# Optimization experiments

Hardware: AMD Instinct MI355X
Metric: run time of the kernel (lower is better)

## Reference

```python
import jax, jax.numpy as jnp
import numpy as np

N_NODES = 100000
N_EDGES = 3200000
F_IN, F_HID, F_OUT = 512, 128, 32


def setup_inputs() -> dict:
    key = jax.random.key(0)
    ks = jax.random.split(key, 8)
    x = jax.random.normal(ks[0], (N_NODES, F_IN), dtype=jnp.float32)
    edge_row = jax.random.randint(ks[1], (N_EDGES,), 0, N_NODES, dtype=jnp.int32)
    edge_col = jax.random.randint(ks[2], (N_EDGES,), 0, N_NODES, dtype=jnp.int32)
    edge_val = jax.random.uniform(ks[3], (N_EDGES,), dtype=jnp.float32)
    W1 = jax.random.normal(ks[4], (F_IN, F_HID), dtype=jnp.float32) / np.sqrt(F_IN)
    b1 = jnp.zeros((F_HID,), dtype=jnp.float32)
    W2 = jax.random.normal(ks[5], (F_HID, F_OUT), dtype=jnp.float32) / np.sqrt(F_HID)
    b2 = jnp.zeros((F_OUT,), dtype=jnp.float32)
    return {"x": x, "edge_row": edge_row, "edge_col": edge_col,
            "edge_val": edge_val, "W1": W1, "b1": b1, "W2": W2, "b2": b2}


def _spmm(edge_row, edge_col, edge_val, dense):
    # out[r] = sum_{e: row[e]==r} val[e] * dense[col[e]]  (COO SpMM)
    gathered = dense[edge_col] * edge_val[:, None]  # [E, F]
    return jax.ops.segment_sum(gathered, edge_row, num_segments=N_NODES)


def reference(x, edge_row, edge_col, edge_val, W1, b1, W2, b2):
    # GraphConvolution 1: support = x@W1; out = A @ support + b1
    h = _spmm(edge_row, edge_col, edge_val, x @ W1) + b1
    h = jax.nn.relu(h)
    # GraphConvolution 2
    logits = _spmm(edge_row, edge_col, edge_val, h @ W2) + b2
    return jax.nn.log_softmax(logits, axis=1)
```

## Files before the change

### kernel.cpp

```cpp
#include <hip/hip_runtime.h>


#define NN 100000
#define NE 3200000
#define FIN 512
#define FHID 128
#define FOUT 32
#define BROWS 256
#define NBUCK 391
#define NPART 256
#define CHUNK 12800
#define TOT (NBUCK * NPART)
#define NSCAN1 98

typedef __attribute__((ext_vector_type(8))) short bf16x8;
typedef __attribute__((ext_vector_type(4))) float f32x4;

static __device__ __forceinline__ unsigned short f2bf(float f) {
    unsigned u = __float_as_uint(f);
    unsigned r = (u + 0x7FFFu + ((u >> 16) & 1u)) >> 16;
    return (unsigned short)r;
}
static __device__ __forceinline__ float bf2f(unsigned short u) {
    return __uint_as_float(((unsigned)u) << 16);
}
static __device__ __forceinline__ float bflo(unsigned u) {
    return __uint_as_float(u << 16);
}
static __device__ __forceinline__ float bfhi(unsigned u) {
    return __uint_as_float(u & 0xffff0000u);
}

__global__ __launch_bounds__(256) void hist_part(const int* __restrict__ erow,
                                                 int* __restrict__ cntG) {
    __shared__ int c[NBUCK];
    const int t = threadIdx.x;
    const int w = blockIdx.x;
    for (int i = t; i < NBUCK; i += 256) c[i] = 0;
    __syncthreads();
    const int e0 = w * CHUNK;
    const int e1 = min(e0 + CHUNK, NE);
    for (int e = e0 + t; e < e1; e += 256) atomicAdd(&c[erow[e] >> 8], 1);
    __syncthreads();
    for (int i = t; i < NBUCK; i += 256) cntG[w * NBUCK + i] = c[i];
}

__global__ __launch_bounds__(256) void scan1_kernel(const int* __restrict__ cntG,
                                                    int* __restrict__ off,
                                                    int* __restrict__ partials) {
    __shared__ int s[256];
    int t = threadIdx.x;
    int i0 = blockIdx.x * 1024 + t * 4;
    int v[4];
#pragma unroll
    for (int j = 0; j < 4; ++j) {
        int i = i0 + j;
        v[j] = (i < TOT) ? cntG[(i & (NPART - 1)) * NBUCK + (i >> 8)] : 0;
    }
    int lsum = v[0] + v[1] + v[2] + v[3];
    s[t] = lsum;
    __syncthreads();
    for (int o = 1; o < 256; o <<= 1) {
        int xv = (t >= o) ? s[t - o] : 0;
        __syncthreads();
        s[t] += xv;
        __syncthreads();
    }
    if (t == 255) partials[blockIdx.x] = s[255];
    int run = s[t] - lsum;
#pragma unroll
    for (int j = 0; j < 4; ++j) {
        if (i0 + j < TOT) off[i0 + j] = run;
        run += v[j];
    }
}

__global__ void scan2_kernel(int* partials) {
    __shared__ int s[128];
    int t = threadIdx.x;
    int v = (t < NSCAN1) ? partials[t] : 0;
    s[t] = v;
    __syncthreads();
    for (int o = 1; o < 128; o <<= 1) {
        int xv = (t >= o) ? s[t - o] : 0;
        __syncthreads();
        s[t] += xv;
        __syncthreads();
    }
    if (t < NSCAN1) partials[t] = s[t] - v;
}

__global__ __launch_bounds__(256) void scan3_kernel(int* __restrict__ off,
                                                    const int* __restrict__ partials) {
    int add = partials[blockIdx.x];
    int i0 = blockIdx.x * 1024 + threadIdx.x * 4;
#pragma unroll
    for (int j = 0; j < 4; ++j)
        if (i0 + j < TOT) off[i0 + j] += add;
}

__global__ void make_bstart(const int* __restrict__ off, int* __restrict__ bstart) {
    int t = blockIdx.x * 256 + threadIdx.x;
    if (t < NBUCK) bstart[t] = off[t * NPART];
    if (t == 0) bstart[NBUCK] = NE;
}

__global__ __launch_bounds__(256) void scatter_part(const int* __restrict__ erow,
                                                    const int* __restrict__ ecol,
                                                    const float* __restrict__ eval,
                                                    const int* __restrict__ off,
                                                    int2* __restrict__ bcolval) {
    __shared__ int pos[NBUCK];
    const int t = threadIdx.x;
    const int w = blockIdx.x;
    for (int b = t; b < NBUCK; b += 256) pos[b] = off[b * NPART + w];
    __syncthreads();
    const int e0 = w * CHUNK;
    const int e1 = min(e0 + CHUNK, NE);
    for (int e = e0 + t; e < e1; e += 256) {
        int r = erow[e];
        int idx = atomicAdd(&pos[r >> 8], 1);
        bcolval[idx] = make_int2(ecol[e] | ((r & 255) << 20), __float_as_int(eval[e]));
    }
}

__global__ __launch_bounds__(256) void bucket_to_csr(const int* __restrict__ bstart,
                                                     const int2* __restrict__ bcolval,
                                                     int* __restrict__ rowptr,
                                                     int2* __restrict__ epack) {
    __shared__ int cnt[256];
    __shared__ int pos[256];
    __shared__ int s[256];
    const int b = blockIdx.x;
    const int t = threadIdx.x;
    const int s0 = bstart[b];
    const int n = bstart[b + 1] - s0;
    cnt[t] = 0;
    __syncthreads();
    for (int i = t; i < n; i += 256)
        atomicAdd(&cnt[((unsigned)bcolval[s0 + i].x) >> 20], 1);
    __syncthreads();
    int myc = cnt[t];
    s[t] = myc;
    __syncthreads();
    for (int o = 1; o < 256; o <<= 1) {
        int xv = (t >= o) ? s[t - o] : 0;
        __syncthreads();
        s[t] += xv;
        __syncthreads();
    }
    int excl = s[t] - myc;
    pos[t] = excl;
    int row = b * BROWS + t;
    if (row < NN) rowptr[row] = s0 + excl;
    if (b == 0 && t == 0) rowptr[NN] = NE;
    __syncthreads();
    for (int i = t; i < n; i += 256) {
        int2 v = bcolval[s0 + i];
        int p = atomicAdd(&pos[((unsigned)v.x) >> 20], 1);
        epack[s0 + p] = make_int2(v.x & 0xFFFFF, v.y);
    }
}

__global__ __launch_bounds__(256) void prep_w1(const float* __restrict__ W1,
                                               unsigned short* __restrict__ W1t) {
    int t = blockIdx.x * 256 + threadIdx.x;
    int n = t & 127;
    int k = t >> 7;
    W1t[n * 512 + k] = f2bf(W1[k * 128 + n]);
}

__global__ __launch_bounds__(256) void gemm1_mfma(const float* __restrict__ x,
                                                  const unsigned short* __restrict__ W1t,
                                                  unsigned short* __restrict__ out) {
    __shared__ __align__(16) unsigned short As[128 * 32];
    const int tid = threadIdx.x;
    const int lane = tid & 63;
    const int w = __builtin_amdgcn_readfirstlane(tid >> 6);
    const int quad = lane >> 4;
    const int m = lane & 15;
    const int row0 = blockIdx.x * 128;

    f32x4 acc[8][2];
#pragma unroll
    for (int mt = 0; mt < 8; ++mt)
#pragma unroll
        for (int nt = 0; nt < 2; ++nt) acc[mt][nt] = (f32x4){0.f, 0.f, 0.f, 0.f};

    int srow[4], skq[4];
    const float* sptr[4];
#pragma unroll
    for (int s = 0; s < 4; ++s) {
        int f = tid + s * 256;
        srow[s] = f >> 3;
        skq[s] = f & 7;
        sptr[s] = x + (size_t)(row0 + srow[s]) * FIN + skq[s] * 4;
    }
    float4 ld[4];
#pragma unroll
    for (int s = 0; s < 4; ++s)
        ld[s] = (row0 + srow[s] < NN) ? *(const float4*)sptr[s]
                                      : make_float4(0.f, 0.f, 0.f, 0.f);

    for (int ks = 0; ks < 16; ++ks) {
        __syncthreads();
#pragma unroll
        for (int s = 0; s < 4; ++s) {
            int r = srow[s], kq = skq[s];
            int mt = r >> 4, mm = r & 15;
            int off = mt * 512 + (kq >> 1) * 128 + mm * 8 + (kq & 1) * 4;
            ushort4 p;
            p.x = f2bf(ld[s].x);
            p.y = f2bf(ld[s].y);
            p.z = f2bf(ld[s].z);
            p.w = f2bf(ld[s].w);
            *(ushort4*)&As[off] = p;
        }
        __syncthreads();
        if (ks < 15) {
#pragma unroll
            for (int s = 0; s < 4; ++s)
                ld[s] = (row0 + srow[s] < NN)
                            ? *(const float4*)(sptr[s] + (ks + 1) * 32)
                            : make_float4(0.f, 0.f, 0.f, 0.f);
        }
        bf16x8 bfr[2];
#pragma unroll
        for (int nt = 0; nt < 2; ++nt) {
            int n = (w * 2 + nt) * 16 + m;
            bfr[nt] = *(const bf16x8*)(W1t + (size_t)n * 512 + ks * 32 + quad * 8);
        }
#pragma unroll
        for (int mt = 0; mt < 8; ++mt) {
            bf16x8 af = *(const bf16x8*)&As[mt * 512 + quad * 128 + m * 8];
            acc[mt][0] = __builtin_amdgcn_mfma_f32_16x16x32_bf16(af, bfr[0], acc[mt][0], 0, 0, 0);
            acc[mt][1] = __builtin_amdgcn_mfma_f32_16x16x32_bf16(af, bfr[1], acc[mt][1], 0, 0, 0);
        }
    }
#pragma unroll
    for (int mt = 0; mt < 8; ++mt)
#pragma unroll
        for (int nt = 0; nt < 2; ++nt) {
            int col = (w * 2 + nt) * 16 + m;
#pragma unroll
            for (int r = 0; r < 4; ++r) {
                int row = row0 + mt * 16 + quad * 4 + r;
                if (row < NN) out[(size_t)row * FHID + col] = f2bf(acc[mt][nt][r]);
            }
        }
}

__global__ __launch_bounds__(256) void spmm1_kernel(const int* __restrict__ rowptr,
                                                    const int2* __restrict__ epack,
                                                    const unsigned short* __restrict__ dense,
                                                    const float* __restrict__ b1,
                                                    unsigned short* __restrict__ h) {
    const int gtid = blockIdx.x * 256 + threadIdx.x;
    const int wid = gtid >> 6;
    const int lane = threadIdx.x & 63;
    const int q = lane >> 4;
    const int sl = lane & 15;
    const int row = wid * 4 + q;
    const int start = rowptr[row];
    const int cnt = rowptr[row + 1] - start;
    float acc[8];
#pragma unroll
    for (int i = 0; i < 8; ++i) acc[i] = 0.f;

    for (int base = 0; base < cnt; base += 16) {
        const int rem = cnt - base;
        int2 p = make_int2(0, 0);
        if (sl < rem) p = epack[start + base + sl];
        const int jn = min(16, rem);
        for (int j = 0; j < jn; j += 4) {
            int cj[4];
            float vj[4];
            uint4 d[4];
#pragma unroll
            for (int k = 0; k < 4; ++k) {
                cj[k] = __shfl(p.x, q * 16 + j + k, 64);
                vj[k] = __shfl(__int_as_float(p.y), q * 16 + j + k, 64);
            }
#pragma unroll
            for (int k = 0; k < 4; ++k)
                d[k] = *(const uint4*)(dense + (size_t)cj[k] * FHID + sl * 8);
#pragma unroll
            for (int k = 0; k < 4; ++k) {
                acc[0] += vj[k] * bflo(d[k].x);
                acc[1] += vj[k] * bfhi(d[k].x);
                acc[2] += vj[k] * bflo(d[k].y);
                acc[3] += vj[k] * bfhi(d[k].y);
                acc[4] += vj[k] * bflo(d[k].z);
                acc[5] += vj[k] * bfhi(d[k].z);
                acc[6] += vj[k] * bflo(d[k].w);
                acc[7] += vj[k] * bfhi(d[k].w);
            }
        }
    }
    float4 bb0 = *(const float4*)(b1 + sl * 8);
    float4 bb1 = *(const float4*)(b1 + sl * 8 + 4);
    uint4 st;
    st.x = (unsigned)f2bf(fmaxf(acc[0] + bb0.x, 0.f)) |
           ((unsigned)f2bf(fmaxf(acc[1] + bb0.y, 0.f)) << 16);
    st.y = (unsigned)f2bf(fmaxf(acc[2] + bb0.z, 0.f)) |
           ((unsigned)f2bf(fmaxf(acc[3] + bb0.w, 0.f)) << 16);
    st.z = (unsigned)f2bf(fmaxf(acc[4] + bb1.x, 0.f)) |
           ((unsigned)f2bf(fmaxf(acc[5] + bb1.y, 0.f)) << 16);
    st.w = (unsigned)f2bf(fmaxf(acc[6] + bb1.z, 0.f)) |
           ((unsigned)f2bf(fmaxf(acc[7] + bb1.w, 0.f)) << 16);
    *(uint4*)(h + (size_t)row * FHID + sl * 8) = st;
}

__global__ __launch_bounds__(256) void gemm2_kernel(const unsigned short* __restrict__ h,
                                                    const float* __restrict__ W2,
                                                    unsigned short* __restrict__ out) {
    __shared__ float hs[64][129];
    const int tid = threadIdx.x;
    const int lane = tid & 63;
    const int cg = __builtin_amdgcn_readfirstlane(tid >> 6);
    const int row0 = blockIdx.x * 64;
    const int row = row0 + lane;

    float acc[8];
#pragma unroll
    for (int c = 0; c < 8; ++c) acc[c] = 0.f;

#pragma unroll
    for (int j = 0; j < 8; ++j) {
        int f4 = tid + j * 256;
        int r = f4 >> 5;
        int kq = f4 & 31;
        ushort4 v = make_ushort4(0, 0, 0, 0);
        if (row0 + r < NN) v = *(const ushort4*)(h + (size_t)(row0 + r) * FHID + kq * 4);
        hs[r][kq * 4 + 0] = bf2f(v.x);
        hs[r][kq * 4 + 1] = bf2f(v.y);
        hs[r][kq * 4 + 2] = bf2f(v.z);
        hs[r][kq * 4 + 3] = bf2f(v.w);
    }
    __syncthreads();
#pragma unroll 4
    for (int k = 0; k < FHID; ++k) {
        float a = hs[lane][k];
        const float* wrow = W2 + k * FOUT + cg * 8;
#pragma unroll
        for (int c = 0; c < 8; ++c) acc[c] += a * wrow[c];
    }
    if (row < NN) {
        uint4 st;
        st.x = (unsigned)f2bf(acc[0]) | ((unsigned)f2bf(acc[1]) << 16);
        st.y = (unsigned)f2bf(acc[2]) | ((unsigned)f2bf(acc[3]) << 16);
        st.z = (unsigned)f2bf(acc[4]) | ((unsigned)f2bf(acc[5]) << 16);
        st.w = (unsigned)f2bf(acc[6]) | ((unsigned)f2bf(acc[7]) << 16);
        *(uint4*)(out + (size_t)row * FOUT + cg * 8) = st;
    }
}

__global__ __launch_bounds__(256) void spmm2_kernel(const int* __restrict__ rowptr,
                                                    const int2* __restrict__ epack,
                                                    const unsigned short* __restrict__ dense,
                                                    const float* __restrict__ b2,
                                                    float* __restrict__ out) {
    const int gtid = blockIdx.x * 256 + threadIdx.x;
    const int wid = gtid >> 6;
    const int lane = threadIdx.x & 63;
    const int o = lane >> 3;
    const int sl = lane & 7;
    const int row = wid * 8 + o;
    const int start = rowptr[row];
    const int cnt = rowptr[row + 1] - start;
    float acc[4];
#pragma unroll
    for (int i = 0; i < 4; ++i) acc[i] = 0.f;

    for (int base = 0; base < cnt; base += 8) {
        const int rem = cnt - base;
        int2 p = make_int2(0, 0);
        if (sl < rem) p = epack[start + base + sl];
        const int jn = min(8, rem);
        for (int j = 0; j < jn; j += 4) {
            int cj[4];
            float vj[4];
            uint2 d[4];
#pragma unroll
            for (int k = 0; k < 4; ++k) {
                cj[k] = __shfl(p.x, o * 8 + j + k, 64);
                vj[k] = __shfl(__int_as_float(p.y), o * 8 + j + k, 64);
            }
#pragma unroll
            for (int k = 0; k < 4; ++k)
                d[k] = *(const uint2*)(dense + (size_t)cj[k] * FOUT + sl * 4);
#pragma unroll
            for (int k = 0; k < 4; ++k) {
                acc[0] += vj[k] * bflo(d[k].x);
                acc[1] += vj[k] * bfhi(d[k].x);
                acc[2] += vj[k] * bflo(d[k].y);
                acc[3] += vj[k] * bfhi(d[k].y);
            }
        }
    }
    float4 bb = *(const float4*)(b2 + sl * 4);
    acc[0] += bb.x;
    acc[1] += bb.y;
    acc[2] += bb.z;
    acc[3] += bb.w;
    float m = fmaxf(fmaxf(acc[0], acc[1]), fmaxf(acc[2], acc[3]));
#pragma unroll
    for (int mask = 4; mask >= 1; mask >>= 1) m = fmaxf(m, __shfl_xor(m, mask, 64));
    float ssum = expf(acc[0] - m) + expf(acc[1] - m) + expf(acc[2] - m) + expf(acc[3] - m);
#pragma unroll
    for (int mask = 4; mask >= 1; mask >>= 1) ssum += __shfl_xor(ssum, mask, 64);
    float lse = m + logf(ssum);
    float4 st = make_float4(acc[0] - lse, acc[1] - lse, acc[2] - lse, acc[3] - lse);
    *(float4*)(out + (size_t)row * FOUT + sl * 4) = st;
}

extern "C" void kernel_launch(void* const* d_in, const int* in_sizes, int n_in,
                              void* d_out, int out_size, void* d_ws, size_t ws_size,
                              hipStream_t stream) {
    const float* x = (const float*)d_in[0];
    const int* erow = (const int*)d_in[1];
    const int* ecol = (const int*)d_in[2];
    const float* eval = (const float*)d_in[3];
    const float* W1 = (const float*)d_in[4];
    const float* b1 = (const float*)d_in[5];
    const float* W2 = (const float*)d_in[6];
    const float* b2 = (const float*)d_in[7];
    float* out = (float*)d_out;

    char* ws = (char*)d_ws;
    size_t off_b = 0;
    auto walloc = [&](size_t bytes) -> void* {
        void* p = ws + off_b;
        off_b = (off_b + bytes + 255) & ~(size_t)255;
        return p;
    };
    int2* epack = (int2*)walloc((size_t)NE * 8);
    int* rowptr = (int*)walloc((size_t)(NN + 1) * 4);
    int* cntG = (int*)walloc((size_t)TOT * 4);
    int* off = (int*)walloc((size_t)TOT * 4);
    int* bstart = (int*)walloc((size_t)(NBUCK + 1) * 4);
    int* partials = (int*)walloc(4096);
    unsigned short* W1t = (unsigned short*)walloc((size_t)FHID * FIN * 2);
    char* uni = (char*)walloc((size_t)NN * FHID * 2 * 2);
    int2* bcolval = (int2*)uni;
    unsigned short* support1 = (unsigned short*)uni;
    unsigned short* h = (unsigned short*)(uni + (size_t)NN * FHID * 2);
    unsigned short* support2 = support1;

    prep_w1<<<256, 256, 0, stream>>>(W1, W1t);
    hist_part<<<NPART, 256, 0, stream>>>(erow, cntG);
    scan1_kernel<<<NSCAN1, 256, 0, stream>>>(cntG, off, partials);
    scan2_kernel<<<1, 128, 0, stream>>>(partials);
    scan3_kernel<<<NSCAN1, 256, 0, stream>>>(off, partials);
    make_bstart<<<2, 256, 0, stream>>>(off, bstart);
    scatter_part<<<NPART, 256, 0, stream>>>(erow, ecol, eval, off, bcolval);
    bucket_to_csr<<<NBUCK, 256, 0, stream>>>(bstart, bcolval, rowptr, epack);

    gemm1_mfma<<<(NN + 127) / 128, 256, 0, stream>>>(x, W1t, support1);
    spmm1_kernel<<<NN / 16, 256, 0, stream>>>(rowptr, epack, support1, b1, h);
    gemm2_kernel<<<(NN + 63) / 64, 256, 0, stream>>>(h, W2, support2);
    spmm2_kernel<<<NN / 32, 256, 0, stream>>>(rowptr, epack, support2, b2, out);
}
```

Before: 646.9 us.

## Fuse prep kernels, merge CSR build with GEMM1, remap SpMM to wave-per-row

Merges the W1 transpose with the edge histogram, removes make_bstart, and runs bucket_to_csr and gemm1 as one launch using disjoint block ranges so they can overlap. Both SpMM kernels now assign one wavefront per row, broadcasting edge indices with readlane and having each lane gather a narrow slice of the dense row. Workspace buffers that used to alias are now allocated separately, which the fusion needs. This trades launch count and idle time for narrower per-lane gathers, and the wave-per-row mapping may waste lanes on low-degree rows.

```diff
diff --git a/kernel.cpp b/kernel.cpp
--- a/kernel.cpp
+++ b/kernel.cpp
@@ -12,6 +12,7 @@
 #define CHUNK 12800
 #define TOT (NBUCK * NPART)
 #define NSCAN1 98
+#define GG1 ((NN + 127) / 128)
 
 typedef __attribute__((ext_vector_type(8))) short bf16x8;
 typedef __attribute__((ext_vector_type(4))) float f32x4;
@@ -31,18 +32,27 @@
     return __uint_as_float(u & 0xffff0000u);
 }
 
-__global__ __launch_bounds__(256) void hist_part(const int* __restrict__ erow,
-                                                 int* __restrict__ cntG) {
-    __shared__ int c[NBUCK];
-    const int t = threadIdx.x;
-    const int w = blockIdx.x;
-    for (int i = t; i < NBUCK; i += 256) c[i] = 0;
-    __syncthreads();
-    const int e0 = w * CHUNK;
-    const int e1 = min(e0 + CHUNK, NE);
-    for (int e = e0 + t; e < e1; e += 256) atomicAdd(&c[erow[e] >> 8], 1);
-    __syncthreads();
-    for (int i = t; i < NBUCK; i += 256) cntG[w * NBUCK + i] = c[i];
+__global__ __launch_bounds__(256) void fused_prep_hist(const float* __restrict__ W1,
+                                                       unsigned short* __restrict__ W1t,
+                                                       const int* __restrict__ erow,
+                                                       int* __restrict__ cntG) {
+    if (blockIdx.x < NPART) {
+        __shared__ int c[NBUCK];
+        const int t = threadIdx.x;
+        const int w = blockIdx.x;
+        for (int i = t; i < NBUCK; i += 256) c[i] = 0;
+        __syncthreads();
+        const int e0 = w * CHUNK;
+        const int e1 = min(e0 + CHUNK, NE);
+        for (int e = e0 + t; e < e1; e += 256) atomicAdd(&c[erow[e] >> 8], 1);
+        __syncthreads();
+        for (int i = t; i < NBUCK; i += 256) cntG[w * NBUCK + i] = c[i];
+    } else {
+        int t = (blockIdx.x - NPART) * 256 + threadIdx.x;
+        int n = t & 127;
+        int k = t >> 7;
+        W1t[n * 512 + k] = f2bf(W1[k * 128 + n]);
+    }
 }
 
 __global__ __launch_bounds__(256) void scan1_kernel(const int* __restrict__ cntG,
@@ -97,12 +107,6 @@
 #pragma unroll
     for (int j = 0; j < 4; ++j)
         if (i0 + j < TOT) off[i0 + j] += add;
-}
-
-__global__ void make_bstart(const int* __restrict__ off, int* __restrict__ bstart) {
-    int t = blockIdx.x * 256 + threadIdx.x;
-    if (t < NBUCK) bstart[t] = off[t * NPART];
-    if (t == 0) bstart[NBUCK] = NE;
 }
 
 __global__ __launch_bounds__(256) void scatter_part(const int* __restrict__ erow,
@@ -124,130 +128,122 @@
     }
 }
 
-__global__ __launch_bounds__(256) void bucket_to_csr(const int* __restrict__ bstart,
-                                                     const int2* __restrict__ bcolval,
-                                                     int* __restrict__ rowptr,
-                                                     int2* __restrict__ epack) {
-    __shared__ int cnt[256];
-    __shared__ int pos[256];
-    __shared__ int s[256];
-    const int b = blockIdx.x;
-    const int t = threadIdx.x;
-    const int s0 = bstart[b];
-    const int n = bstart[b + 1] - s0;
-    cnt[t] = 0;
-    __syncthreads();
-    for (int i = t; i < n; i += 256)
-        atomicAdd(&cnt[((unsigned)bcolval[s0 + i].x) >> 20], 1);
-    __syncthreads();
-    int myc = cnt[t];
-    s[t] = myc;
-    __syncthreads();
-    for (int o = 1; o < 256; o <<= 1) {
-        int xv = (t >= o) ? s[t - o] : 0;
-        __syncthreads();
-        s[t] += xv;
-        __syncthreads();
-    }
-    int excl = s[t] - myc;
-    pos[t] = excl;
-    int row = b * BROWS + t;
-    if (row < NN) rowptr[row] = s0 + excl;
-    if (b == 0 && t == 0) rowptr[NN] = NE;
-    __syncthreads();
-    for (int i = t; i < n; i += 256) {
-        int2 v = bcolval[s0 + i];
-        int p = atomicAdd(&pos[((unsigned)v.x) >> 20], 1);
-        epack[s0 + p] = make_int2(v.x & 0xFFFFF, v.y);
-    }
-}
-
-__global__ __launch_bounds__(256) void prep_w1(const float* __restrict__ W1,
-                                               unsigned short* __restrict__ W1t) {
-    int t = blockIdx.x * 256 + threadIdx.x;
-    int n = t & 127;
-    int k = t >> 7;
-    W1t[n * 512 + k] = f2bf(W1[k * 128 + n]);
-}
-
-__global__ __launch_bounds__(256) void gemm1_mfma(const float* __restrict__ x,
-                                                  const unsigned short* __restrict__ W1t,
-                                                  unsigned short* __restrict__ out) {
-    __shared__ __align__(16) unsigned short As[128 * 32];
-    const int tid = threadIdx.x;
-    const int lane = tid & 63;
-    const int w = __builtin_amdgcn_readfirstlane(tid >> 6);
-    const int quad = lane >> 4;
-    const int m = lane & 15;
-    const int row0 = blockIdx.x * 128;
-
-    f32x4 acc[8][2];
-#pragma unroll
-    for (int mt = 0; mt < 8; ++mt)
-#pragma unroll
-        for (int nt = 0; nt < 2; ++nt) acc[mt][nt] = (f32x4){0.f, 0.f, 0.f, 0.f};
-
-    int srow[4], skq[4];
-    const float* sptr[4];
-#pragma unroll
-    for (int s = 0; s < 4; ++s) {
-        int f = tid + s * 256;
-        srow[s] = f >> 3;
-        skq[s] = f & 7;
-        sptr[s] = x + (size_t)(row0 + srow[s]) * FIN + skq[s] * 4;
-    }
-    float4 ld[4];
-#pragma unroll
-    for (int s = 0; s < 4; ++s)
-        ld[s] = (row0 + srow[s] < NN) ? *(const float4*)sptr[s]
-                                      : make_float4(0.f, 0.f, 0.f, 0.f);
-
-    for (int ks = 0; ks < 16; ++ks) {
-        __syncthreads();
+__global__ __launch_bounds__(256) void fused_csr_gemm1(
+    const int* __restrict__ off, const int2* __restrict__ bcolval,
+    int* __restrict__ rowptr, int2* __restrict__ epack,
+    const float* __restrict__ x, const unsigned short* __restrict__ W1t,
+    unsigned short* __restrict__ outd) {
+    if (blockIdx.x < GG1) {
+        __shared__ __align__(16) unsigned short As[128 * 32];
+        const int tid = threadIdx.x;
+        const int lane = tid & 63;
+        const int w = __builtin_amdgcn_readfirstlane(tid >> 6);
+        const int quad = lane >> 4;
+        const int m = lane & 15;
+        const int row0 = blockIdx.x * 128;
+
+        f32x4 acc[8][2];
+#pragma unroll
+        for (int mt = 0; mt < 8; ++mt)
+#pragma unroll
+            for (int nt = 0; nt < 2; ++nt) acc[mt][nt] = (f32x4){0.f, 0.f, 0.f, 0.f};
+
+        int srow[4], skq[4];
+        const float* sptr[4];
 #pragma unroll
         for (int s = 0; s < 4; ++s) {
-            int r = srow[s], kq = skq[s];
-            int mt = r >> 4, mm = r & 15;
-            int off = mt * 512 + (kq >> 1) * 128 + mm * 8 + (kq & 1) * 4;
-            ushort4 p;
-            p.x = f2bf(ld[s].x);
-            p.y = f2bf(ld[s].y);
-            p.z = f2bf(ld[s].z);
-            p.w = f2bf(ld[s].w);
-            *(ushort4*)&As[off] = p;
-        }
-        __syncthreads();
-        if (ks < 15) {
-#pragma unroll
-            for (int s = 0; s < 4; ++s)
-                ld[s] = (row0 + srow[s] < NN)
-                            ? *(const float4*)(sptr[s] + (ks + 1) * 32)
-                            : make_float4(0.f, 0.f, 0.f, 0.f);
-        }
-        bf16x8 bfr[2];
-#pragma unroll
-        for (int nt = 0; nt < 2; ++nt) {
-            int n = (w * 2 + nt) * 16 + m;
-            bfr[nt] = *(const bf16x8*)(W1t + (size_t)n * 512 + ks * 32 + quad * 8);
-        }
-#pragma unroll
-        for (int mt = 0; mt < 8; ++mt) {
-            bf16x8 af = *(const bf16x8*)&As[mt * 512 + quad * 128 + m * 8];
-            acc[mt][0] = __builtin_amdgcn_mfma_f32_16x16x32_bf16(af, bfr[0], acc[mt][0], 0, 0, 0);
-            acc[mt][1] = __builtin_amdgcn_mfma_f32_16x16x32_bf16(af, bfr[1], acc[mt][1], 0, 0, 0);
-        }
-    }
-#pragma unroll
-    for (int mt = 0; mt < 8; ++mt)
-#pragma unroll
-        for (int nt = 0; nt < 2; ++nt) {
-            int col = (w * 2 + nt) * 16 + m;
-#pragma unroll
-            for (int r = 0; r < 4; ++r) {
-                int row = row0 + mt * 16 + quad * 4 + r;
-                if (row < NN) out[(size_t)row * FHID + col] = f2bf(acc[mt][nt][r]);
+            int f = tid + s * 256;
+            srow[s] = f >> 3;
+            skq[s] = f & 7;
+            sptr[s] = x + (size_t)(row0 + srow[s]) * FIN + skq[s] * 4;
+        }
+        float4 ld[4];
+#pragma unroll
+        for (int s = 0; s < 4; ++s)
+            ld[s] = (row0 + srow[s] < NN) ? *(const float4*)sptr[s]
+                                          : make_float4(0.f, 0.f, 0.f, 0.f);
+
+        for (int ks = 0; ks < 16; ++ks) {
+            __syncthreads();
+#pragma unroll
+            for (int s = 0; s < 4; ++s) {
+                int r = srow[s], kq = skq[s];
+                int mt = r >> 4, mm = r & 15;
+                int offs = mt * 512 + (kq >> 1) * 128 + mm * 8 + (kq & 1) * 4;
+                ushort4 p;
+                p.x = f2bf(ld[s].x);
+                p.y = f2bf(ld[s].y);
+                p.z = f2bf(ld[s].z);
+                p.w = f2bf(ld[s].w);
+                *(ushort4*)&As[offs] = p;
             }
-        }
+            __syncthreads();
+            if (ks < 15) {
+#pragma unroll
+                for (int s = 0; s < 4; ++s)
+                    ld[s] = (row0 + srow[s] < NN)
+                                ? *(const float4*)(sptr[s] + (ks + 1) * 32)
+                                : make_float4(0.f, 0.f, 0.f, 0.f);
+            }
+            bf16x8 bfr[2];
+#pragma unroll
+            for (int nt = 0; nt < 2; ++nt) {
+                int n = (w * 2 + nt) * 16 + m;
+                bfr[nt] = *(const bf16x8*)(W1t + (size_t)n * 512 + ks * 32 + quad * 8);
+            }
+#pragma unroll
+            for (int mt = 0; mt < 8; ++mt) {
+                bf16x8 af = *(const bf16x8*)&As[mt * 512 + quad * 128 + m * 8];
+                acc[mt][0] = __builtin_amdgcn_mfma_f32_16x16x32_bf16(af, bfr[0], acc[mt][0], 0, 0, 0);
+                acc[mt][1] = __builtin_amdgcn_mfma_f32_16x16x32_bf16(af, bfr[1], acc[mt][1], 0, 0, 0);
+            }
+        }
+#pragma unroll
+        for (int mt = 0; mt < 8; ++mt)
+#pragma unroll
+            for (int nt = 0; nt < 2; ++nt) {
+                int col = (w * 2 + nt) * 16 + m;
+#pragma unroll
+                for (int r = 0; r < 4; ++r) {
+                    int row = row0 + mt * 16 + quad * 4 + r;
+                    if (row < NN) outd[(size_t)row * FHID + col] = f2bf(acc[mt][nt][r]);
+                }
+            }
+    } else {
+        __shared__ int cnt[256];
+        __shared__ int pos[256];
+        __shared__ int s[256];
+        const int b = blockIdx.x - GG1;
+        const int t = threadIdx.x;
+        const int s0 = off[b * NPART];
+        const int send = (b == NBUCK - 1) ? NE : off[(b + 1) * NPART];
+        const int n = send - s0;
+        cnt[t] = 0;
+        __syncthreads();
+        for (int i = t; i < n; i += 256)
+            atomicAdd(&cnt[((unsigned)bcolval[s0 + i].x) >> 20], 1);
+        __syncthreads();
+        int myc = cnt[t];
+        s[t] = myc;
+        __syncthreads();
+        for (int o = 1; o < 256; o <<= 1) {
+            int xv = (t >= o) ? s[t - o] : 0;
+            __syncthreads();
+            s[t] += xv;
+            __syncthreads();
+        }
+        int excl = s[t] - myc;
+        pos[t] = excl;
+        int row = b * BROWS + t;
+        if (row < NN) rowptr[row] = s0 + excl;
+        if (b == 0 && t == 0) rowptr[NN] = NE;
+        __syncthreads();
+        for (int i = t; i < n; i += 256) {
+            int2 v = bcolval[s0 + i];
+            int p = atomicAdd(&pos[((unsigned)v.x) >> 20], 1);
+            epack[s0 + p] = make_int2(v.x & 0xFFFFF, v.y);
+        }
+    }
 }
 
 __global__ __launch_bounds__(256) void spmm1_kernel(const int* __restrict__ rowptr,
@@ -255,60 +251,36 @@
                                                     const unsigned short* __restrict__ dense,
                                                     const float* __restrict__ b1,
                                                     unsigned short* __restrict__ h) {
-    const int gtid = blockIdx.x * 256 + threadIdx.x;
-    const int wid = gtid >> 6;
     const int lane = threadIdx.x & 63;
-    const int q = lane >> 4;
-    const int sl = lane & 15;
-    const int row = wid * 4 + q;
-    const int start = rowptr[row];
-    const int cnt = rowptr[row + 1] - start;
-    float acc[8];
-#pragma unroll
-    for (int i = 0; i < 8; ++i) acc[i] = 0.f;
-
-    for (int base = 0; base < cnt; base += 16) {
-        const int rem = cnt - base;
-        int2 p = make_int2(0, 0);
-        if (sl < rem) p = epack[start + base + sl];
-        const int jn = min(16, rem);
-        for (int j = 0; j < jn; j += 4) {
-            int cj[4];
-            float vj[4];
-            uint4 d[4];
-#pragma unroll
-            for (int k = 0; k < 4; ++k) {
-                cj[k] = __shfl(p.x, q * 16 + j + k, 64);
-                vj[k] = __shfl(__int_as_float(p.y), q * 16 + j + k, 64);
-            }
-#pragma unroll
-            for (int k = 0; k < 4; ++k)
-                d[k] = *(const uint4*)(dense + (size_t)cj[k] * FHID + sl * 8);
-#pragma unroll
-            for (int k = 0; k < 4; ++k) {
-                acc[0] += vj[k] * bflo(d[k].x);
-                acc[1] += vj[k] * bfhi(d[k].x);
-                acc[2] += vj[k] * bflo(d[k].y);
-                acc[3] += vj[k] * bfhi(d[k].y);
-                acc[4] += vj[k] * bflo(d[k].z);
-                acc[5] += vj[k] * bfhi(d[k].z);
-                acc[6] += vj[k] * bflo(d[k].w);
-                acc[7] += vj[k] * bfhi(d[k].w);
-            }
-        }
-    }
-    float4 bb0 = *(const float4*)(b1 + sl * 8);
-    float4 bb1 = *(const float4*)(b1 + sl * 8 + 4);
-    uint4 st;
-    st.x = (unsigned)f2bf(fmaxf(acc[0] + bb0.x, 0.f)) |
-           ((unsigned)f2bf(fmaxf(acc[1] + bb0.y, 0.f)) << 16);
-    st.y = (unsigned)f2bf(fmaxf(acc[2] + bb0.z, 0.f)) |
-           ((unsigned)f2bf(fmaxf(acc[3] + bb0.w, 0.f)) << 16);
-    st.z = (unsigned)f2bf(fmaxf(acc[4] + bb1.x, 0.f)) |
-           ((unsigned)f2bf(fmaxf(acc[5] + bb1.y, 0.f)) << 16);
-    st.w = (unsigned)f2bf(fmaxf(acc[6] + bb1.z, 0.f)) |
-           ((unsigned)f2bf(fmaxf(acc[7] + bb1.w, 0.f)) << 16);
-    *(uint4*)(h + (size_t)row * FHID + sl * 8) = st;
+    const int row = blockIdx.x * 4 + (threadIdx.x >> 6);
+    const int start = __builtin_amdgcn_readfirstlane(rowptr[row]);
+    const int cnt = __builtin_amdgcn_readfirstlane(rowptr[row + 1]) - start;
+    const int sl16 = lane & 15;
+    float acc0 = 0.f, acc1 = 0.f;
+
+    for (int j = 0; j < cnt; j += 16) {
+        int idx = j + sl16;
+        idx = idx < cnt ? idx : cnt - 1;
+        const int2 p = epack[start + idx];
+        const int rem = cnt - j;
+        unsigned d[16];
+#pragma unroll
+        for (int k = 0; k < 16; ++k) {
+            int col = __builtin_amdgcn_readlane(p.x, k);
+            col = (k < rem) ? col : 0;
+            d[k] = *((const unsigned*)(dense + ((size_t)col << 7)) + lane);
+        }
+#pragma unroll
+        for (int k = 0; k < 16; ++k) {
+            float v = (k < rem) ? __int_as_float(__builtin_amdgcn_readlane(p.y, k)) : 0.f;
+            acc0 = fmaf(v, bflo(d[k]), acc0);
+            acc1 = fmaf(v, bfhi(d[k]), acc1);
+        }
+    }
+    float2 bb = *(const float2*)(b1 + lane * 2);
+    unsigned r0 = f2bf(fmaxf(acc0 + bb.x, 0.f));
+    unsigned r1 = f2bf(fmaxf(acc1 + bb.y, 0.f));
+    *((unsigned*)(h + (size_t)row * FHID) + lane) = r0 | (r1 << 16);
 }
 
 __global__ __launch_bounds__(256) void gemm2_kernel(const unsigned short* __restrict__ h,
@@ -360,58 +332,49 @@
                                                     const unsigned short* __restrict__ dense,
                                                     const float* __restrict__ b2,
                                                     float* __restrict__ out) {
-    const int gtid = blockIdx.x * 256 + threadIdx.x;
-    const int wid = gtid >> 6;
     const int lane = threadIdx.x & 63;
-    const int o = lane >> 3;
-    const int sl = lane & 7;
-    const int row = wid * 8 + o;
-    const int start = rowptr[row];
-    const int cnt = rowptr[row + 1] - start;
-    float acc[4];
-#pragma unroll
-    for (int i = 0; i < 4; ++i) acc[i] = 0.f;
-
-    for (int base = 0; base < cnt; base += 8) {
-        const int rem = cnt - base;
-        int2 p = make_int2(0, 0);
-        if (sl < rem) p = epack[start + base + sl];
-        const int jn = min(8, rem);
-        for (int j = 0; j < jn; j += 4) {
-            int cj[4];
-            float vj[4];
-            uint2 d[4];
-#pragma unroll
-            for (int k = 0; k < 4; ++k) {
-                cj[k] = __shfl(p.x, o * 8 + j + k, 64);
-                vj[k] = __shfl(__int_as_float(p.y), o * 8 + j + k, 64);
-            }
-#pragma unroll
-            for (int k = 0; k < 4; ++k)
-                d[k] = *(const uint2*)(dense + (size_t)cj[k] * FOUT + sl * 4);
-#pragma unroll
-            for (int k = 0; k < 4; ++k) {
-                acc[0] += vj[k] * bflo(d[k].x);
-                acc[1] += vj[k] * bfhi(d[k].x);
-                acc[2] += vj[k] * bflo(d[k].y);
-                acc[3] += vj[k] * bfhi(d[k].y);
-            }
-        }
-    }
-    float4 bb = *(const float4*)(b2 + sl * 4);
-    acc[0] += bb.x;
-    acc[1] += bb.y;
-    acc[2] += bb.z;
-    acc[3] += bb.w;
-    float m = fmaxf(fmaxf(acc[0], acc[1]), fmaxf(acc[2], acc[3]));
-#pragma unroll
-    for (int mask = 4; mask >= 1; mask >>= 1) m = fmaxf(m, __shfl_xor(m, mask, 64));
-    float ssum = expf(acc[0] - m) + expf(acc[1] - m) + expf(acc[2] - m) + expf(acc[3] - m);
-#pragma unroll
-    for (int mask = 4; mask >= 1; mask >>= 1) ssum += __shfl_xor(ssum, mask, 64);
+    const int row = blockIdx.x * 4 + (threadIdx.x >> 6);
+    const int start = __builtin_amdgcn_readfirstlane(rowptr[row]);
+    const int cnt = __builtin_amdgcn_readfirstlane(rowptr[row + 1]) - start;
+    const int col = lane & 31;
+    const int slot = lane >> 5;
+    const int sl16 = lane & 15;
+    float acc = 0.f;
+
+    for (int j = 0; j < cnt; j += 16) {
+        int idx = j + sl16;
+        idx = idx < cnt ? idx : cnt - 1;
+        const int2 p = epack[start + idx];
+        const int rem = cnt - j;
+        unsigned short d[8];
+        float vv[8];
+#pragma unroll
+        for (int k = 0; k < 8; ++k) {
+            int cA = __builtin_amdgcn_readlane(p.x, 2 * k);
+            int cB = __builtin_amdgcn_readlane(p.x, 2 * k + 1);
+            int ei = 2 * k + slot;
+            int c = slot ? cB : cA;
+            c = (ei < rem) ? c : 0;
+            d[k] = *(dense + (size_t)c * FOUT + col);
+            int vA = __builtin_amdgcn_readlane(p.y, 2 * k);
+            int vB = __builtin_amdgcn_readlane(p.y, 2 * k + 1);
+            float v = __int_as_float(slot ? vB : vA);
+            vv[k] = (ei < rem) ? v : 0.f;
+        }
+#pragma unroll
+        for (int k = 0; k < 8; ++k) acc = fmaf(vv[k], bf2f(d[k]), acc);
+    }
+    acc += __shfl_xor(acc, 32, 64);
+    acc += b2[col];
+    float m = acc;
+#pragma unroll
+    for (int mask = 16; mask >= 1; mask >>= 1) m = fmaxf(m, __shfl_xor(m, mask, 64));
+    float ex = expf(acc - m);
+    float ssum = ex;
+#pragma unroll
+    for (int mask = 16; mask >= 1; mask >>= 1) ssum += __shfl_xor(ssum, mask, 64);
     float lse = m + logf(ssum);
-    float4 st = make_float4(acc[0] - lse, acc[1] - lse, acc[2] - lse, acc[3] - lse);
-    *(float4*)(out + (size_t)row * FOUT + sl * 4) = st;
+    if (lane < 32) out[(size_t)row * FOUT + col] = acc - lse;
 }
 
 extern "C" void kernel_launch(void* const* d_in, const int* in_sizes, int n_in,
@@ -438,26 +401,21 @@
     int* rowptr = (int*)walloc((size_t)(NN + 1) * 4);
     int* cntG = (int*)walloc((size_t)TOT * 4);
     int* off = (int*)walloc((size_t)TOT * 4);
-    int* bstart = (int*)walloc((size_t)(NBUCK + 1) * 4);
     int* partials = (int*)walloc(4096);
     unsigned short* W1t = (unsigned short*)walloc((size_t)FHID * FIN * 2);
-    char* uni = (char*)walloc((size_t)NN * FHID * 2 * 2);
-    int2* bcolval = (int2*)uni;
-    unsigned short* support1 = (unsigned short*)uni;
-    unsigned short* h = (unsigned short*)(uni + (size_t)NN * FHID * 2);
+    int2* bcolval = (int2*)walloc((size_t)NE * 8);
+    unsigned short* support1 = (unsigned short*)walloc((size_t)NN * FHID * 2);
+    unsigned short* h = (unsigned short*)walloc((size_t)NN * FHID * 2);
     unsigned short* support2 = support1;
 
-    prep_w1<<<256, 256, 0, stream>>>(W1, W1t);
-    hist_part<<<NPART, 256, 0, stream>>>(erow, cntG);
+    fused_prep_hist<<<NPART + 256, 256, 0, stream>>>(W1, W1t, erow, cntG);
     scan1_kernel<<<NSCAN1, 256, 0, stream>>>(cntG, off, partials);
     scan2_kernel<<<1, 128, 0, stream>>>(partials);
     scan3_kernel<<<NSCAN1, 256, 0, stream>>>(off, partials);
-    make_bstart<<<2, 256, 0, stream>>>(off, bstart);
     scatter_part<<<NPART, 256, 0, stream>>>(erow, ecol, eval, off, bcolval);
-    bucket_to_csr<<<NBUCK, 256, 0, stream>>>(bstart, bcolval, rowptr, epack);
-
-    gemm1_mfma<<<(NN + 127) / 128, 256, 0, stream>>>(x, W1t, support1);
-    spmm1_kernel<<<NN / 16, 256, 0, stream>>>(rowptr, epack, support1, b1, h);
+    fused_csr_gemm1<<<GG1 + NBUCK, 256, 0, stream>>>(off, bcolval, rowptr, epack,
+                                                     x, W1t, support1);
+    spmm1_kernel<<<NN / 4, 256, 0, stream>>>(rowptr, epack, support1, b1, h);
     gemm2_kernel<<<(NN + 63) / 64, 256, 0, stream>>>(h, W2, support2);
-    spmm2_kernel<<<NN / 32, 256, 0, stream>>>(rowptr, epack, support2, b2, out);
-}
+    spmm2_kernel<<<NN / 4, 256, 0, stream>>>(rowptr, epack, support2, b2, out);
+}
```

New measurement: 662.3 us. 1.02x slower.
